# Kernel tuning notes

Measured on AMD Instinct MI355X. Metric: run time of the kernel, lower is better.

Reference implementation:

```python
import jax, jax.numpy as jnp
import numpy as np

N_SRC = 100_000   # hetero[s].num_nodes
N_DST = 100_000   # hetero[d].num_nodes
E     = 800_000   # edge_index.size(1)
D_SRC = 256       # node_dims['src']
D_DST = 256       # node_dims['dst']
D_REL = 128       # d_rel


def setup_inputs() -> dict:
    key = jax.random.key(0)
    ks = jax.random.split(key, 6)
    x_src = jax.random.normal(ks[0], (N_SRC, D_SRC), jnp.float32)
    x_dst = jax.random.normal(ks[1], (N_DST, D_DST), jnp.float32)
    # nn.Linear(d_in, d_rel, bias=False) weights, stored transposed as [d_in, d_rel]
    W_src = jax.random.normal(ks[2], (D_SRC, D_REL), jnp.float32) / np.sqrt(D_SRC).astype(np.float32)
    W_dst = jax.random.normal(ks[3], (D_DST, D_REL), jnp.float32) / np.sqrt(D_DST).astype(np.float32)
    edge_src = jax.random.randint(ks[4], (E,), 0, N_SRC, jnp.int32)  # edge_index[0]
    edge_dst = jax.random.randint(ks[5], (E,), 0, N_DST, jnp.int32)  # edge_index[1]
    return {"x_src": x_src, "x_dst": x_dst, "W_src": W_src, "W_dst": W_dst,
            "edge_src": edge_src, "edge_dst": edge_dst}


def reference(x_src, x_dst, W_src, W_dst, edge_src, edge_dst):
    # Per-type linear projection (bias-free), as in self.proj[nt](feats)
    p_src = x_src @ W_src            # [N_src, d_rel]
    p_dst = x_dst @ W_dst            # projected per module, unused by this edge type
    del p_dst

    # Degree of each destination (A.sum(dim=1)), clamped to >= 1.
    deg = jax.ops.segment_sum(jnp.ones((E,), jnp.float32), edge_dst,
                              num_segments=N_DST)
    deg = jnp.maximum(deg, 1.0)      # [N_dst]

    # Degree-normalized SpMM: sum of source features per destination / deg.
    # (coalescing duplicate edges sums their unit values; segment_sum matches.)
    agg = jax.ops.segment_sum(p_src[edge_src], edge_dst,
                              num_segments=N_DST)            # [N_dst, d_rel]
    dst = agg / deg[:, None]

    # rel_embs[et] = {'dst': dst, 'src_in': x_proj[s], 'deg_dst': deg}
    return dst, p_src, deg
```

## Files before the change

### kernel.cpp

```cpp
#include <hip/hip_runtime.h>
#include <hip/hip_bf16.h>

#define D_SRC 256
#define D_REL 128

typedef __bf16 bf16x8 __attribute__((ext_vector_type(8)));
typedef float f32x4 __attribute__((ext_vector_type(4)));
typedef float f32x2 __attribute__((ext_vector_type(2)));

typedef const __attribute__((address_space(1))) void GASV;
typedef __attribute__((address_space(3))) void LASV;

__global__ __launch_bounds__(64) void prep_w_kernel(const float* __restrict__ W,
                                                    bf16x8* __restrict__ Wt,
                                                    int* __restrict__ deg_i, int ndeg) {
    int c = blockIdx.x;
    int ks = c >> 3, n = c & 7;
    int lane = threadIdx.x;
    int col = n * 16 + (lane & 15);
    int k0 = ks * 32 + (lane >> 4) * 8;
    bf16x8 v;
#pragma unroll
    for (int j = 0; j < 8; ++j) v[j] = (__bf16)W[(size_t)(k0 + j) * D_REL + col];
    Wt[c * 64 + lane] = v;
    for (int i = blockIdx.x * 64 + lane; i < ndeg; i += 64 * 64) deg_i[i] = 0;
}

__global__ __launch_bounds__(256, 4) void proj_count_kernel(
    const float* __restrict__ x, const f32x4* __restrict__ Wt,
    float* __restrict__ out_f32, unsigned short* __restrict__ out_bf, int M,
    const int* __restrict__ edge_dst, int* __restrict__ deg_i,
    int* __restrict__ pos_arr, int E, int nproj, int ncb) {
    __shared__ float xlds[32 * 256];
    int tid = threadIdx.x;

    if (blockIdx.x >= nproj) {
        int cb = blockIdx.x - nproj;
        int stride = ncb * 256;
        for (int e = cb * 256 + tid; e < E; e += stride)
            pos_arr[e] = atomicAdd(&deg_i[edge_dst[e]], 1);
        return;
    }

    int wid = tid >> 6, lane = tid & 63;
    int r = lane & 15, kq = lane >> 4;
    int row0 = blockIdx.x * 32;

#pragma unroll
    for (int j = 0; j < 8; ++j) {
        int rl = wid * 8 + j;
        int grow = min(row0 + rl, M - 1);
        const float* src = x + (size_t)grow * D_SRC + ((lane ^ j) << 2);
        __builtin_amdgcn_global_load_lds((GASV*)src, (LASV*)&xlds[rl * 256], 16, 0, 0);
    }

    f32x4 wfv[2][8];
#pragma unroll
    for (int s = 0; s < 2; ++s)
#pragma unroll
        for (int ks = 0; ks < 8; ++ks)
            wfv[s][ks] = Wt[(ks * 8 + wid * 2 + s) * 64 + lane];
#pragma unroll
    for (int s = 0; s < 2; ++s)
#pragma unroll
        for (int ks = 0; ks < 8; ++ks)
            asm volatile("" : "+v"(wfv[s][ks]));

    __syncthreads();

    f32x4 acc[2][2];
#pragma unroll
    for (int t = 0; t < 2; ++t)
#pragma unroll
        for (int s = 0; s < 2; ++s) acc[t][s] = (f32x4)(0.f);

    const f32x4* xl = (const f32x4*)xlds;
    int r8 = r & 7;
#pragma unroll
    for (int ks = 0; ks < 8; ++ks) {
        int q0 = ks * 8 + kq * 2;
#pragma unroll
        for (int t = 0; t < 2; ++t) {
            int rl = t * 16 + r;
            f32x4 a0 = xl[rl * 64 + (q0 ^ r8)];
            f32x4 a1 = xl[rl * 64 + ((q0 + 1) ^ r8)];
            bf16x8 xf;
            xf[0] = (__bf16)a0[0]; xf[1] = (__bf16)a0[1];
            xf[2] = (__bf16)a0[2]; xf[3] = (__bf16)a0[3];
            xf[4] = (__bf16)a1[0]; xf[5] = (__bf16)a1[1];
            xf[6] = (__bf16)a1[2]; xf[7] = (__bf16)a1[3];
            acc[t][0] = __builtin_amdgcn_mfma_f32_16x16x32_bf16(
                __builtin_bit_cast(bf16x8, wfv[0][ks]), xf, acc[t][0], 0, 0, 0);
            acc[t][1] = __builtin_amdgcn_mfma_f32_16x16x32_bf16(
                __builtin_bit_cast(bf16x8, wfv[1][ks]), xf, acc[t][1], 0, 0, 0);
        }
    }

    int col0 = wid * 32;
#pragma unroll
    for (int t = 0; t < 2; ++t) {
        int prow = row0 + t * 16 + r;
        if (prow < M) {
            size_t o0 = (size_t)prow * D_REL + col0 + kq * 4;
            __builtin_nontemporal_store(acc[t][0], (f32x4*)(out_f32 + o0));
            __builtin_nontemporal_store(acc[t][1], (f32x4*)(out_f32 + o0 + 16));
            ushort4 b0, b1;
            b0.x = __bfloat16_as_ushort(__float2bfloat16(acc[t][0][0]));
            b0.y = __bfloat16_as_ushort(__float2bfloat16(acc[t][0][1]));
            b0.z = __bfloat16_as_ushort(__float2bfloat16(acc[t][0][2]));
            b0.w = __bfloat16_as_ushort(__float2bfloat16(acc[t][0][3]));
            b1.x = __bfloat16_as_ushort(__float2bfloat16(acc[t][1][0]));
            b1.y = __bfloat16_as_ushort(__float2bfloat16(acc[t][1][1]));
            b1.z = __bfloat16_as_ushort(__float2bfloat16(acc[t][1][2]));
            b1.w = __bfloat16_as_ushort(__float2bfloat16(acc[t][1][3]));
            *(ushort4*)(out_bf + o0) = b0;
            *(ushort4*)(out_bf + o0 + 16) = b1;
        }
    }
}

__global__ __launch_bounds__(1024) void scan_blocks(
    const int* __restrict__ deg_i, int* __restrict__ incl,
    int* __restrict__ bsums, int n) {
    int i = blockIdx.x * 1024 + threadIdx.x;
    int v = (i < n) ? deg_i[i] : 0;
    int lane = threadIdx.x & 63;
    int wid = threadIdx.x >> 6;
    int x = v;
#pragma unroll
    for (int off = 1; off < 64; off <<= 1) {
        int y = __shfl_up(x, off, 64);
        if (lane >= off) x += y;
    }
    __shared__ int wsum[16];
    if (lane == 63) wsum[wid] = x;
    __syncthreads();
    if (wid == 0 && lane < 16) {
        int s = wsum[lane];
#pragma unroll
        for (int off = 1; off < 16; off <<= 1) {
            int y = __shfl_up(s, off, 64);
            if (lane >= off) s += y;
        }
        wsum[lane] = s;
    }
    __syncthreads();
    int add = (wid > 0) ? wsum[wid - 1] : 0;
    x += add;
    if (i < n) incl[i] = x;
    if (threadIdx.x == 1023) bsums[blockIdx.x] = x;
}

__global__ __launch_bounds__(1024) void finalize_kernel(
    const int* __restrict__ deg_i, const int* __restrict__ incl,
    const int* __restrict__ bsums, int* __restrict__ row_start,
    float* __restrict__ deg_out, int n, int E) {
    __shared__ int soff;
    int bid = blockIdx.x;
    if (threadIdx.x < 64) {
        int lane = threadIdx.x;
        int s = 0;
        for (int i = lane; i < bid; i += 64) s += bsums[i];
#pragma unroll
        for (int m = 32; m >= 1; m >>= 1) s += __shfl_xor(s, m, 64);
        if (lane == 0) soff = s;
    }
    __syncthreads();
    int off = soff;
    int i = bid * 1024 + threadIdx.x;
    if (i < n) {
        row_start[i] = off + incl[i] - deg_i[i];
        deg_out[i] = (float)max(deg_i[i], 1);
    }
    if (i == 0) row_start[n] = E;
}

__global__ void fill_kernel(const int* __restrict__ edge_src,
                            const int* __restrict__ edge_dst,
                            const int* __restrict__ row_start,
                            const int* __restrict__ pos_arr,
                            int* __restrict__ bucket, int E) {
    int e = blockIdx.x * 256 + threadIdx.x;
    if (e < E) {
        int d = edge_dst[e];
        bucket[row_start[d] + pos_arr[e]] = edge_src[e];
    }
}

__global__ __launch_bounds__(256) void gather_kernel(
    const unsigned int* __restrict__ p_bf, const int* __restrict__ row_start,
    const int* __restrict__ bucket, const float* __restrict__ deg_out,
    float* __restrict__ dst, int n) {
    int row = blockIdx.x * 4 + (threadIdx.x >> 6);
    int lane = threadIdx.x & 63;
    if (row >= n) return;
    int beg = row_start[row], end = row_start[row + 1];
    float ax = 0.f, ay = 0.f;
    int idx = beg;
    for (; idx + 8 <= end; idx += 8) {
        int s[8];
        unsigned int v[8];
#pragma unroll
        for (int u = 0; u < 8; ++u) s[u] = bucket[idx + u];
#pragma unroll
        for (int u = 0; u < 8; ++u) v[u] = p_bf[(size_t)s[u] * 64 + lane];
#pragma unroll
        for (int u = 0; u < 8; ++u) {
            ax += __uint_as_float(v[u] << 16);
            ay += __uint_as_float(v[u] & 0xffff0000u);
        }
    }
    for (; idx + 4 <= end; idx += 4) {
        int s0 = bucket[idx + 0], s1 = bucket[idx + 1];
        int s2 = bucket[idx + 2], s3 = bucket[idx + 3];
        unsigned int v0 = p_bf[(size_t)s0 * 64 + lane];
        unsigned int v1 = p_bf[(size_t)s1 * 64 + lane];
        unsigned int v2 = p_bf[(size_t)s2 * 64 + lane];
        unsigned int v3 = p_bf[(size_t)s3 * 64 + lane];
        ax += __uint_as_float(v0 << 16) + __uint_as_float(v1 << 16)
            + __uint_as_float(v2 << 16) + __uint_as_float(v3 << 16);
        ay += __uint_as_float(v0 & 0xffff0000u) + __uint_as_float(v1 & 0xffff0000u)
            + __uint_as_float(v2 & 0xffff0000u) + __uint_as_float(v3 & 0xffff0000u);
    }
    for (; idx < end; ++idx) {
        int s = bucket[idx];
        unsigned int v = p_bf[(size_t)s * 64 + lane];
        ax += __uint_as_float(v << 16);
        ay += __uint_as_float(v & 0xffff0000u);
    }
    float dinv = 1.0f / deg_out[row];
    f32x2 o;
    o[0] = ax * dinv;
    o[1] = ay * dinv;
    f32x2* dp = (f32x2*)dst + (size_t)row * 64 + lane;
    __builtin_nontemporal_store(o, dp);
}

extern "C" void kernel_launch(void* const* d_in, const int* in_sizes, int n_in,
                              void* d_out, int out_size, void* d_ws, size_t ws_size,
                              hipStream_t stream) {
    const float* x_src = (const float*)d_in[0];
    const float* W_src = (const float*)d_in[2];
    const int* edge_src = (const int*)d_in[4];
    const int* edge_dst = (const int*)d_in[5];

    const int N_SRC = in_sizes[0] / D_SRC;
    const int N_DST = in_sizes[1] / D_SRC;
    const int E = in_sizes[4];

    float* out_dst = (float*)d_out;
    float* out_psrc = out_dst + (size_t)N_DST * D_REL;
    float* out_deg = out_psrc + (size_t)N_SRC * D_REL;

    int* deg_i = (int*)d_ws;
    int* incl = deg_i + N_DST;
    int* row_start = incl + N_DST;
    int* bsums = row_start + N_DST + 1;
    int* pos_arr = bsums + 128;
    int* bucket = pos_arr + E;
    size_t int_bytes = (size_t)(3 * N_DST + 1 + 128 + 2 * (size_t)E) * sizeof(int);
    size_t wt_off = (int_bytes + 255) & ~(size_t)255;
    bf16x8* Wt = (bf16x8*)((char*)d_ws + wt_off);
    size_t pbf_off = wt_off + 65536;
    unsigned short* p_bf = (unsigned short*)((char*)d_ws + pbf_off);

    prep_w_kernel<<<64, 64, 0, stream>>>(W_src, Wt, deg_i, N_DST);
    {
        int nproj = (N_SRC + 31) / 32;
        int ncb = 768;
        proj_count_kernel<<<nproj + ncb, 256, 0, stream>>>(
            x_src, (const f32x4*)Wt, out_psrc, p_bf, N_SRC,
            edge_dst, deg_i, pos_arr, E, nproj, ncb);
    }
    int nb = (N_DST + 1023) / 1024;
    scan_blocks<<<nb, 1024, 0, stream>>>(deg_i, incl, bsums, N_DST);
    finalize_kernel<<<nb, 1024, 0, stream>>>(deg_i, incl, bsums, row_start, out_deg, N_DST, E);
    fill_kernel<<<(E + 255) / 256, 256, 0, stream>>>(edge_src, edge_dst, row_start, pos_arr, bucket, E);
    gather_kernel<<<(N_DST + 3) / 4, 256, 0, stream>>>(
        (const unsigned int*)p_bf, row_start, bucket, out_deg, out_dst, N_DST);
}
```

Baseline: 134.5 us.

## Split count from GEMM and fuse scan with finalize via decoupled lookback

Moves the edge-degree atomic counting out of the projection GEMM launch into its own kernel, so the GEMM kernel no longer carries the extra count blocks. Merges the two-pass scan and finalize into one kernel: each block publishes its total to bsums with a release store, then spins with acquire loads on earlier blocks' sums, which removes one launch and the incl array round trip. The spin wait assumes earlier blocks are scheduled, which holds for the ~98 blocks here. Separating count from GEMM gives up the earlier overlap of atomics with GEMM work.

```diff
diff --git a/kernel.cpp b/kernel.cpp
--- a/kernel.cpp
+++ b/kernel.cpp
@@ -13,7 +13,8 @@
 
 __global__ __launch_bounds__(64) void prep_w_kernel(const float* __restrict__ W,
                                                     bf16x8* __restrict__ Wt,
-                                                    int* __restrict__ deg_i, int ndeg) {
+                                                    int* __restrict__ deg_i, int ndeg,
+                                                    int* __restrict__ bsums) {
     int c = blockIdx.x;
     int ks = c >> 3, n = c & 7;
     int lane = threadIdx.x;
@@ -24,24 +25,21 @@
     for (int j = 0; j < 8; ++j) v[j] = (__bf16)W[(size_t)(k0 + j) * D_REL + col];
     Wt[c * 64 + lane] = v;
     for (int i = blockIdx.x * 64 + lane; i < ndeg; i += 64 * 64) deg_i[i] = 0;
-}
-
-__global__ __launch_bounds__(256, 4) void proj_count_kernel(
+    if (blockIdx.x == 0)
+        for (int i = lane; i < 128; i += 64) bsums[i] = -1;
+}
+
+__global__ void count_kernel(const int* __restrict__ edge_dst, int* __restrict__ deg_i,
+                             int* __restrict__ pos_arr, int E) {
+    int e = blockIdx.x * 256 + threadIdx.x;
+    if (e < E) pos_arr[e] = atomicAdd(&deg_i[edge_dst[e]], 1);
+}
+
+__global__ __launch_bounds__(256, 4) void proj_gemm_kernel(
     const float* __restrict__ x, const f32x4* __restrict__ Wt,
-    float* __restrict__ out_f32, unsigned short* __restrict__ out_bf, int M,
-    const int* __restrict__ edge_dst, int* __restrict__ deg_i,
-    int* __restrict__ pos_arr, int E, int nproj, int ncb) {
+    float* __restrict__ out_f32, unsigned short* __restrict__ out_bf, int M) {
     __shared__ float xlds[32 * 256];
     int tid = threadIdx.x;
-
-    if (blockIdx.x >= nproj) {
-        int cb = blockIdx.x - nproj;
-        int stride = ncb * 256;
-        for (int e = cb * 256 + tid; e < E; e += stride)
-            pos_arr[e] = atomicAdd(&deg_i[edge_dst[e]], 1);
-        return;
-    }
-
     int wid = tid >> 6, lane = tid & 63;
     int r = lane & 15, kq = lane >> 4;
     int row0 = blockIdx.x * 32;
@@ -119,10 +117,11 @@
     }
 }
 
-__global__ __launch_bounds__(1024) void scan_blocks(
-    const int* __restrict__ deg_i, int* __restrict__ incl,
-    int* __restrict__ bsums, int n) {
-    int i = blockIdx.x * 1024 + threadIdx.x;
+__global__ __launch_bounds__(1024) void scanfin_kernel(
+    const int* __restrict__ deg_i, int* __restrict__ bsums,
+    int* __restrict__ row_start, float* __restrict__ deg_out, int n, int E) {
+    int bid = blockIdx.x;
+    int i = bid * 1024 + threadIdx.x;
     int v = (i < n) ? deg_i[i] : 0;
     int lane = threadIdx.x & 63;
     int wid = threadIdx.x >> 6;
@@ -133,6 +132,7 @@
         if (lane >= off) x += y;
     }
     __shared__ int wsum[16];
+    __shared__ int soff;
     if (lane == 63) wsum[wid] = x;
     __syncthreads();
     if (wid == 0 && lane < 16) {
@@ -147,30 +147,25 @@
     __syncthreads();
     int add = (wid > 0) ? wsum[wid - 1] : 0;
     x += add;
-    if (i < n) incl[i] = x;
-    if (threadIdx.x == 1023) bsums[blockIdx.x] = x;
-}
-
-__global__ __launch_bounds__(1024) void finalize_kernel(
-    const int* __restrict__ deg_i, const int* __restrict__ incl,
-    const int* __restrict__ bsums, int* __restrict__ row_start,
-    float* __restrict__ deg_out, int n, int E) {
-    __shared__ int soff;
-    int bid = blockIdx.x;
+    if (threadIdx.x == 1023)
+        __hip_atomic_store(&bsums[bid], x, __ATOMIC_RELEASE, __HIP_MEMORY_SCOPE_AGENT);
     if (threadIdx.x < 64) {
-        int lane = threadIdx.x;
         int s = 0;
-        for (int i = lane; i < bid; i += 64) s += bsums[i];
+        for (int j = (int)threadIdx.x; j < bid; j += 64) {
+            int w;
+            do {
+                w = __hip_atomic_load(&bsums[j], __ATOMIC_ACQUIRE, __HIP_MEMORY_SCOPE_AGENT);
+            } while (w == -1);
+            s += w;
+        }
 #pragma unroll
         for (int m = 32; m >= 1; m >>= 1) s += __shfl_xor(s, m, 64);
-        if (lane == 0) soff = s;
-    }
-    __syncthreads();
-    int off = soff;
-    int i = bid * 1024 + threadIdx.x;
+        if (threadIdx.x == 0) soff = s;
+    }
+    __syncthreads();
     if (i < n) {
-        row_start[i] = off + incl[i] - deg_i[i];
-        deg_out[i] = (float)max(deg_i[i], 1);
+        row_start[i] = soff + x - v;
+        deg_out[i] = (float)max(v, 1);
     }
     if (i == 0) row_start[n] = E;
 }
@@ -264,17 +259,12 @@
     size_t pbf_off = wt_off + 65536;
     unsigned short* p_bf = (unsigned short*)((char*)d_ws + pbf_off);
 
-    prep_w_kernel<<<64, 64, 0, stream>>>(W_src, Wt, deg_i, N_DST);
-    {
-        int nproj = (N_SRC + 31) / 32;
-        int ncb = 768;
-        proj_count_kernel<<<nproj + ncb, 256, 0, stream>>>(
-            x_src, (const f32x4*)Wt, out_psrc, p_bf, N_SRC,
-            edge_dst, deg_i, pos_arr, E, nproj, ncb);
-    }
+    prep_w_kernel<<<64, 64, 0, stream>>>(W_src, Wt, deg_i, N_DST, bsums);
+    count_kernel<<<(E + 255) / 256, 256, 0, stream>>>(edge_dst, deg_i, pos_arr, E);
+    proj_gemm_kernel<<<(N_SRC + 31) / 32, 256, 0, stream>>>(
+        x_src, (const f32x4*)Wt, out_psrc, p_bf, N_SRC);
     int nb = (N_DST + 1023) / 1024;
-    scan_blocks<<<nb, 1024, 0, stream>>>(deg_i, incl, bsums, N_DST);
-    finalize_kernel<<<nb, 1024, 0, stream>>>(deg_i, incl, bsums, row_start, out_deg, N_DST, E);
+    scanfin_kernel<<<nb, 1024, 0, stream>>>(deg_i, bsums, row_start, out_deg, N_DST, E);
     fill_kernel<<<(E + 255) / 256, 256, 0, stream>>>(edge_src, edge_dst, row_start, pos_arr, bucket, E);
     gather_kernel<<<(N_DST + 3) / 4, 256, 0, stream>>>(
         (const unsigned int*)p_bf, row_start, bucket, out_deg, out_dst, N_DST);
```

Measured after the change: 141.2 us. 1.05x slower.
